# Kernel tuning notes

Hardware: AMD Instinct MI355X
Metric: run time of the kernel (lower is better)

The kernel has to match this reference:

```python
import jax, jax.numpy as jnp
import numpy as np

N = 1_000_000   # mesh points
D_IN = 5        # scalar invariants
H = 128         # hidden width
L = 5           # hidden layers
NB = 10         # tensor bases

# t0 generator basis rows (flattened 3x3 deviatoric diag tensors)
T01 = np.array([-1/3, 0, 0, 0, 1/6, 0, 0, 0, 1/6], dtype=np.float32)
T02 = np.array([1/6, 0, 0, 0, -1/3, 0, 0, 0, 1/6], dtype=np.float32)
T03 = np.array([1/6, 0, 0, 0, 1/6, 0, 0, 0, -1/3], dtype=np.float32)


def _linear_params(k, fan_in, fan_out):
    # xavier_uniform_ with gain=1.0, bias filled with 0.01 (as in init_w_and_b)
    limit = float(np.sqrt(6.0 / (fan_in + fan_out)))
    W = jax.random.uniform(k, (fan_in, fan_out), jnp.float32, -limit, limit)
    b = jnp.full((fan_out,), 0.01, jnp.float32)
    return W, b


def setup_inputs() -> dict:
    key = jax.random.key(0)
    ks = jax.random.split(key, 16)
    x = jax.random.normal(ks[0], (N, D_IN), jnp.float32)
    tb = jax.random.normal(ks[1], (N, NB, 9), jnp.float32)
    inp = {"x": x, "tb": tb}
    dims = [D_IN] + [H] * L
    for i in range(L):
        W, b = _linear_params(ks[2 + i], dims[i], dims[i + 1])
        inp[f"W{i+1}"] = W
        inp[f"b{i+1}"] = b
    inp["Wc"], inp["bc"] = _linear_params(ks[2 + L], H, NB)
    inp["Wg1"], inp["bg1"] = _linear_params(ks[3 + L], H, 1)
    inp["Wg2"], inp["bg2"] = _linear_params(ks[4 + L], H, 1)
    inp["Wg3"], inp["bg3"] = _linear_params(ks[5 + L], H, 1)
    return inp


def reference(x, tb, W1, b1, W2, b2, W3, b3, W4, b4, W5, b5,
              Wc, bc, Wg1, bg1, Wg2, bg2, Wg3, bg3):
    h = x
    for W, b in ((W1, b1), (W2, b2), (W3, b3), (W4, b4), (W5, b5)):
        h = jax.nn.relu(h @ W + b)          # [N, H]
    coeffs = h @ Wc + bc                     # [N, NB]
    g1 = h @ Wg1 + bg1                       # [N, 1]
    g2 = h @ Wg2 + bg2
    g3 = h @ Wg3 + bg3
    t0 = g1 * jnp.asarray(T01) + g2 * jnp.asarray(T02) + g3 * jnp.asarray(T03)  # [N, 9]
    # batched tensor-basis contraction replacing the per-point double loop
    bij = t0 + jnp.einsum('nt,ntc->nc', coeffs, tb)  # [N, 9]
    return bij
```

## Files before the change

### kernel.cpp

```cpp
#include <hip/hip_runtime.h>
#include <stdint.h>


#define NPTS   1000000
#define TPB    512
#define NBLKS  256
#define PTILE  256
#define NT     ((NPTS + PTILE - 1) / PTILE)

typedef uint32_t u32;
typedef __attribute__((ext_vector_type(4)))  u32   u32x4;
typedef __attribute__((ext_vector_type(8)))  short s16x8;
typedef __attribute__((ext_vector_type(16))) float f32x16;
typedef __attribute__((ext_vector_type(4), aligned(4))) float f32x4u;

#define WS_L(l)   ((l)*65536)
#define WS_TAIL   262144
#define WS_W1     (262144 + 8192)
#define WS_BIAS   (262144 + 12288)

#define LDS_BUF0   0
#define LDS_BUF1   65536
#define LDS_HEADS  131072
#define LDS_W1     (131072 + 8192)
#define LDS_BIAS   (131072 + 12288)
#define LDS_TOTAL  147456

#define MFMA(a,b,c) __builtin_amdgcn_mfma_f32_32x32x16_bf16((a),(b),(c),0,0,0)
#define BC16(v)     __builtin_bit_cast(s16x8, (v))

__device__ __forceinline__ u32 cvtpk(float lo, float hi) {
    u32 r;
    asm("v_cvt_pk_bf16_f32 %0, %1, %2" : "=v"(r) : "v"(lo), "v"(hi));
    return r;
}
__device__ __forceinline__ float lo2f(u32 p){ return __builtin_bit_cast(float, p << 16); }
__device__ __forceinline__ float hi2f(u32 p){ return __builtin_bit_cast(float, p & 0xffff0000u); }
__device__ __forceinline__ uint16_t f2bf(float f) {
    u32 u = __builtin_bit_cast(u32, f);
    return (uint16_t)((u + 0x7fffu + ((u >> 16) & 1u)) >> 16);
}
__device__ __forceinline__ float b2f(uint16_t h){ return __builtin_bit_cast(float, (u32)h << 16); }

__device__ __forceinline__ void stageN(const char* g, char* l, int tid, int nbytes) {
    const int w = tid >> 6, ln = tid & 63;
    const char* gp = g + w*1024 + ln*16;
    char* lp = l + w*1024;
    #pragma unroll
    for (int i = 0; i < 8; ++i) {
        if (i*8192 >= nbytes) break;
        __builtin_amdgcn_global_load_lds(
            (const __attribute__((address_space(1))) uint32_t*)(gp + i*8192),
            (__attribute__((address_space(3))) uint32_t*)(lp + i*8192), 16, 0, 0);
    }
}

extern "C" __global__ void __launch_bounds__(256)
tbnn_prep(const float* __restrict__ W1, const float* __restrict__ b1,
          const float* __restrict__ W2, const float* __restrict__ b2,
          const float* __restrict__ W3, const float* __restrict__ b3,
          const float* __restrict__ W4, const float* __restrict__ b4,
          const float* __restrict__ W5, const float* __restrict__ b5,
          const float* __restrict__ Wc, const float* __restrict__ bc,
          const float* __restrict__ Wg1,const float* __restrict__ bg1,
          const float* __restrict__ Wg2,const float* __restrict__ bg2,
          const float* __restrict__ Wg3,const float* __restrict__ bg3,
          char* __restrict__ ws)
{
    int idx = blockIdx.x*256 + threadIdx.x;
    if (idx < 65536) {
        int l = idx >> 14, r = idx & 16383, ifc = r >> 7, of = r & 127;
        const float* Wt = (l==0)?W2:(l==1)?W3:(l==2)?W4:W5;
        float w = Wt[ifc*128 + of];
        uint16_t hb = f2bf(w);
        uint16_t lb = f2bf(w - b2f(hb));
        char* row = ws + WS_L(l) + of*512;
        int o = (2*ifc) ^ ((of&15)<<4);
        *(uint16_t*)(row + o)       = hb;
        *(uint16_t*)(row + 256 + o) = lb;
    } else if (idx < 65536 + 2048) {
        int j = idx - 65536, of = j >> 7, ifc = j & 127;
        float v = 0.f;
        if      (of < 10)  v = Wc[ifc*10 + of];
        else if (of == 10) v = Wg1[ifc];
        else if (of == 11) v = Wg2[ifc];
        else if (of == 12) v = Wg3[ifc];
        uint16_t hb = f2bf(v);
        uint16_t lb = f2bf(v - b2f(hb));
        char* row = ws + WS_TAIL + of*512;
        int o = (2*ifc) ^ ((of&15)<<4);
        *(uint16_t*)(row + o)       = hb;
        *(uint16_t*)(row + 256 + o) = lb;
    } else if (idx < 65536 + 2048 + 128) {
        int of = idx - (65536 + 2048);
        uint16_t* dst = (uint16_t*)(ws + WS_W1 + of*32);
        #pragma unroll
        for (int s = 0; s < 5; ++s) {
            float w = W1[s*128 + of];
            uint16_t hb = f2bf(w);
            dst[s]      = hb;
            dst[6 + s]  = f2bf(w - b2f(hb));
            dst[11 + s] = hb;
        }
        dst[5] = f2bf(b1[of]);
    } else if (idx < 65536 + 2048 + 128 + 544) {
        int j = idx - (65536 + 2048 + 128);
        float v = 0.f;
        if (j < 512) {
            int l = j >> 7, of = j & 127;
            const float* bt = (l==0)?b2:(l==1)?b3:(l==2)?b4:b5;
            v = bt[of];
        } else {
            int of = j - 512;
            if      (of < 10)  v = bc[of];
            else if (of == 10) v = bg1[0];
            else if (of == 11) v = bg2[0];
            else if (of == 12) v = bg3[0];
        }
        *(uint16_t*)(ws + WS_BIAS + j*2) = f2bf(v);
    }
}

#define LAYER(lc, BUFOFF) do {                                                   \
    const char* wb = smem + (BUFOFF);                                            \
    __builtin_amdgcn_s_setprio(1);                                               \
    _Pragma("unroll")                                                            \
    for (int k = 0; k < 8; ++k) {                                                \
        int so = (k*32 + hib) ^ sm;                                              \
        const char* rp = wb + col*512 + so;                                      \
        u32x4 H0 = *(const u32x4*)(rp);                                          \
        u32x4 L0v = *(const u32x4*)(rp + 256);                                   \
        u32x4 H1 = *(const u32x4*)(rp + 32*512);                                 \
        u32x4 L1v = *(const u32x4*)(rp + 32*512 + 256);                          \
        u32x4 H2 = *(const u32x4*)(rp + 64*512);                                 \
        u32x4 L2v = *(const u32x4*)(rp + 64*512 + 256);                          \
        u32x4 H3 = *(const u32x4*)(rp + 96*512);                                 \
        u32x4 L3v = *(const u32x4*)(rp + 96*512 + 256);                          \
        s16x8 bl = BC16(Bl[k]), bh = BC16(Bh[k]);                                \
        acc[0] = MFMA(BC16(H0), bl, (k==0)?zf:acc[0]);                           \
        acc[1] = MFMA(BC16(H1), bl, (k==0)?zf:acc[1]);                           \
        acc[2] = MFMA(BC16(H2), bl, (k==0)?zf:acc[2]);                           \
        acc[3] = MFMA(BC16(H3), bl, (k==0)?zf:acc[3]);                           \
        acc[0] = MFMA(BC16(H0), bh, acc[0]);                                     \
        acc[1] = MFMA(BC16(H1), bh, acc[1]);                                     \
        acc[2] = MFMA(BC16(H2), bh, acc[2]);                                     \
        acc[3] = MFMA(BC16(H3), bh, acc[3]);                                     \
        acc[0] = MFMA(BC16(L0v), bh, acc[0]);                                    \
        acc[1] = MFMA(BC16(L1v), bh, acc[1]);                                    \
        acc[2] = MFMA(BC16(L2v), bh, acc[2]);                                    \
        acc[3] = MFMA(BC16(L3v), bh, acc[3]);                                    \
    }                                                                            \
    _Pragma("unroll")                                                            \
    for (int ot = 0; ot < 4; ++ot) {                                             \
        u32 bw = (u32)*(const uint16_t*)(smem + LDS_BIAS + ((lc)*128 + ot*32 + col)*2); \
        u32x4 Ab; Ab[0] = hi ? 0u : bw; Ab[1]=0u; Ab[2]=0u; Ab[3]=0u;            \
        acc[ot] = MFMA(BC16(Ab), BC16(Bc), acc[ot]);                             \
    }                                                                            \
    __builtin_amdgcn_s_setprio(0);                                               \
    convert();                                                                   \
} while (0)

extern "C" __global__ void __launch_bounds__(TPB)
tbnn_main(const float* __restrict__ x, const float* __restrict__ tb,
          const char* __restrict__ ws, float* __restrict__ out)
{
    extern __shared__ char smem[];
    const int tid  = threadIdx.x;
    const int wave = tid >> 6;
    const int lane = tid & 63;
    const int col  = lane & 31;
    const int hi   = lane >> 5;
    const int sm   = (col & 15) << 4;
    const int hib  = hi * 16;

    stageN(ws + WS_TAIL, smem + LDS_HEADS, tid, 16384);
    stageN(ws + WS_L(0), smem + LDS_BUF0,  tid, 65536);
    stageN(ws + WS_L(1), smem + LDS_BUF1,  tid, 65536);
    __syncthreads();

    u32x4 Bc; Bc[0] = hi ? 0u : 0x00003F80u; Bc[1]=0u; Bc[2]=0u; Bc[3]=0u;
    f32x16 zf;
    #pragma unroll
    for (int i = 0; i < 16; ++i) zf[i] = 0.f;

    for (int t = blockIdx.x; t < NT; t += gridDim.x) {
        const int pb = t*PTILE + wave*32;
        const int p  = pb + col;

        f32x16 acc[4];
        u32x4  Bh[8], Bl[8];

        auto convert = [&]() {
            #pragma unroll
            for (int ot = 0; ot < 4; ++ot) {
                f32x16 a = acc[ot];
                #pragma unroll
                for (int h2 = 0; h2 < 2; ++h2) {
                    float e0 = fmaxf(a[8*h2+0], 0.f), e1 = fmaxf(a[8*h2+1], 0.f);
                    float e2 = fmaxf(a[8*h2+2], 0.f), e3 = fmaxf(a[8*h2+3], 0.f);
                    float e4 = fmaxf(a[8*h2+4], 0.f), e5 = fmaxf(a[8*h2+5], 0.f);
                    float e6 = fmaxf(a[8*h2+6], 0.f), e7 = fmaxf(a[8*h2+7], 0.f);
                    u32 h01 = cvtpk(e0,e1), h23 = cvtpk(e2,e3);
                    u32 h45 = cvtpk(e4,e5), h67 = cvtpk(e6,e7);
                    u32 l01 = cvtpk(e0 - lo2f(h01), e1 - hi2f(h01));
                    u32 l23 = cvtpk(e2 - lo2f(h23), e3 - hi2f(h23));
                    u32 l45 = cvtpk(e4 - lo2f(h45), e5 - hi2f(h45));
                    u32 l67 = cvtpk(e6 - lo2f(h67), e7 - hi2f(h67));
                    auto sh1 = __builtin_amdgcn_permlane32_swap(h01, h45, false, false);
                    auto sh2 = __builtin_amdgcn_permlane32_swap(h23, h67, false, false);
                    u32x4 fh; fh[0]=sh1[0]; fh[1]=sh2[0]; fh[2]=sh1[1]; fh[3]=sh2[1];
                    Bh[2*ot+h2] = fh;
                    auto sl1 = __builtin_amdgcn_permlane32_swap(l01, l45, false, false);
                    auto sl2 = __builtin_amdgcn_permlane32_swap(l23, l67, false, false);
                    u32x4 fl; fl[0]=sl1[0]; fl[1]=sl2[0]; fl[2]=sl1[1]; fl[3]=sl2[1];
                    Bl[2*ot+h2] = fl;
                }
            }
        };

        {
            float x0=0.f,x1=0.f,x2=0.f,x3=0.f,x4=0.f;
            if (p < NPTS) {
                const float* xp = x + (size_t)p*5;
                f32x4u v = *(const f32x4u*)xp;
                x0=v.x; x1=v.y; x2=v.z; x3=v.w; x4=xp[4];
            }
            float h0 = lo2f(cvtpk(x0,x0)), l0 = x0 - h0;
            float h1 = lo2f(cvtpk(x1,x1)), l1 = x1 - h1;
            float h2 = lo2f(cvtpk(x2,x2)), l2 = x2 - h2;
            float h3 = lo2f(cvtpk(x3,x3)), l3 = x3 - h3;
            float h4 = lo2f(cvtpk(x4,x4)), l4 = x4 - h4;
            u32x4 Bx;
            if (hi == 0) {
                Bx[0] = cvtpk(h0,h1); Bx[1] = cvtpk(h2,h3);
                Bx[2] = cvtpk(h4,1.0f); Bx[3] = cvtpk(h0,h1);
            } else {
                Bx[0] = cvtpk(h2,h3); Bx[1] = cvtpk(h4,l0);
                Bx[2] = cvtpk(l1,l2); Bx[3] = cvtpk(l3,l4);
            }
            #pragma unroll
            for (int ot = 0; ot < 4; ++ot) {
                u32x4 Av = *(const u32x4*)(smem + LDS_W1 + (ot*32+col)*32 + hib);
                acc[ot] = MFMA(BC16(Av), BC16(Bx), zf);
            }
        }
        convert();

        LAYER(0, LDS_BUF0);
        __syncthreads();
        stageN(ws + WS_L(2), smem + LDS_BUF0, tid, 65536);
        LAYER(1, LDS_BUF1);
        __syncthreads();
        stageN(ws + WS_L(3), smem + LDS_BUF1, tid, 65536);
        LAYER(2, LDS_BUF0);
        __syncthreads();
        stageN(ws + WS_L(0), smem + LDS_BUF0, tid, 65536);
        LAYER(3, LDS_BUF1);
        __syncthreads();
        stageN(ws + WS_L(1), smem + LDS_BUF1, tid, 65536);

        f32x16 hA, hB;
        __builtin_amdgcn_s_setprio(1);
        #pragma unroll
        for (int k = 0; k < 8; ++k) {
            int so = (k*32 + hib) ^ sm;
            const char* rp = smem + LDS_HEADS + (col&15)*512;
            u32x4 HH = *(const u32x4*)(rp + so);
            u32x4 HL = *(const u32x4*)(rp + 256 + so);
            s16x8 bl = BC16(Bl[k]), bh = BC16(Bh[k]);
            if (k & 1) {
                hB = MFMA(BC16(HH), bl, (k==1)?zf:hB);
                hB = MFMA(BC16(HH), bh, hB);
                hB = MFMA(BC16(HL), bh, hB);
            } else {
                hA = MFMA(BC16(HH), bl, (k==0)?zf:hA);
                hA = MFMA(BC16(HH), bh, hA);
                hA = MFMA(BC16(HL), bh, hA);
            }
        }
        {
            u32 bw = (u32)*(const uint16_t*)(smem + LDS_BIAS + (512 + col)*2);
            u32x4 Ab; Ab[0] = hi ? 0u : bw; Ab[1]=0u; Ab[2]=0u; Ab[3]=0u;
            hA = MFMA(BC16(Ab), BC16(Bc), hA);
        }
        __builtin_amdgcn_s_setprio(0);
        f32x16 h6 = hA + hB;

        if (p < NPTS) {
            const float* tbp = tb + (size_t)p*90;
            f32x16 c = h6;
            const float sixth = 0.16666666666666666f;
            const float third = 0.3333333333333333f;
            float s[9];
            if (hi == 0) {
                float g1 = c[6], g2 = c[7];
                s[0] = -g1*third + g2*sixth;
                s[4] =  g1*sixth - g2*third;
                s[8] =  g1*sixth + g2*sixth;
            } else {
                float g3 = c[4];
                s[0] =  g3*sixth;
                s[4] =  g3*sixth;
                s[8] = -g3*third;
            }
            s[1]=s[2]=s[3]=s[5]=s[6]=s[7]=0.f;
            #pragma unroll
            for (int j = 0; j < 4; ++j) {
                int trow = (hi ? 4 : 0) + j;
                float cf = c[j];
                const float* r = tbp + trow*9;
                f32x4u r0 = *(const f32x4u*)(r);
                f32x4u r1 = *(const f32x4u*)(r + 4);
                float r8 = r[8];
                s[0] += cf*r0.x; s[1] += cf*r0.y; s[2] += cf*r0.z; s[3] += cf*r0.w;
                s[4] += cf*r1.x; s[5] += cf*r1.y; s[6] += cf*r1.z; s[7] += cf*r1.w;
                s[8] += cf*r8;
            }
            if (hi == 0) {
                #pragma unroll
                for (int j = 4; j < 6; ++j) {
                    int trow = 4 + j;
                    float cf = c[j];
                    const float* r = tbp + trow*9;
                    f32x4u r0 = *(const f32x4u*)(r);
                    f32x4u r1 = *(const f32x4u*)(r + 4);
                    float r8 = r[8];
                    s[0] += cf*r0.x; s[1] += cf*r0.y; s[2] += cf*r0.z; s[3] += cf*r0.w;
                    s[4] += cf*r1.x; s[5] += cf*r1.y; s[6] += cf*r1.z; s[7] += cf*r1.w;
                    s[8] += cf*r8;
                }
            }
            #pragma unroll
            for (int j = 0; j < 9; ++j) {
                u32 uv = __builtin_bit_cast(u32, s[j]);
                auto rr = __builtin_amdgcn_permlane32_swap(uv, uv, false, false);
                s[j] = __builtin_bit_cast(float, (u32)rr[0]) + __builtin_bit_cast(float, (u32)rr[1]);
            }
            if (hi == 0) {
                float* op = out + (size_t)p*9;
                f32x4u o0, o1;
                o0.x=s[0]; o0.y=s[1]; o0.z=s[2]; o0.w=s[3];
                o1.x=s[4]; o1.y=s[5]; o1.z=s[6]; o1.w=s[7];
                *(f32x4u*)op       = o0;
                *(f32x4u*)(op + 4) = o1;
                op[8] = s[8];
            }
        }
    }
    __syncthreads();
}

extern "C" void kernel_launch(void* const* d_in, const int* in_sizes, int n_in,
                              void* d_out, int out_size, void* d_ws, size_t ws_size,
                              hipStream_t stream) {
    (void)in_sizes; (void)n_in; (void)out_size; (void)ws_size;
    char* ws = (char*)d_ws;
    hipLaunchKernelGGL(tbnn_prep, dim3(267), dim3(256), 0, stream,
        (const float*)d_in[2],  (const float*)d_in[3],
        (const float*)d_in[4],  (const float*)d_in[5],
        (const float*)d_in[6],  (const float*)d_in[7],
        (const float*)d_in[8],  (const float*)d_in[9],
        (const float*)d_in[10], (const float*)d_in[11],
        (const float*)d_in[12], (const float*)d_in[13],
        (const float*)d_in[14], (const float*)d_in[15],
        (const float*)d_in[16], (const float*)d_in[17],
        (const float*)d_in[18], (const float*)d_in[19],
        ws);
    (void)hipFuncSetAttribute((const void*)tbnn_main,
                              hipFuncAttributeMaxDynamicSharedMemorySize, LDS_TOTAL);
    hipLaunchKernelGGL(tbnn_main, dim3(NBLKS), dim3(TPB), LDS_TOTAL, stream,
        (const float*)d_in[0], (const float*)d_in[1], ws, (float*)d_out);
}
```

Measured before the change: 413.3 us.

## Process two 32-point sub-tiles per wave to amortize weight restaging

Each wave now handles 64 points per tile (two 32-point groups with separate bf16 hi/lo activation buffers), doubling PTILE to 512. Every staged layer weight buffer is reused across both groups, so the per-tile global-to-LDS restaging of all four 64KB hidden-layer weights and the matching barriers happen half as often per point. The heads GEMM also drops its two-accumulator split and uses a single chain. In exchange, register pressure roughly doubles for the activation operands, which may cause spills or lower occupancy at 512 threads per block.

```diff
diff --git a/kernel.cpp b/kernel.cpp
--- a/kernel.cpp
+++ b/kernel.cpp
@@ -5,7 +5,7 @@
 #define NPTS   1000000
 #define TPB    512
 #define NBLKS  256
-#define PTILE  256
+#define PTILE  512
 #define NT     ((NPTS + PTILE - 1) / PTILE)
 
 typedef uint32_t u32;
@@ -121,45 +121,6 @@
     }
 }
 
-#define LAYER(lc, BUFOFF) do {                                                   \
-    const char* wb = smem + (BUFOFF);                                            \
-    __builtin_amdgcn_s_setprio(1);                                               \
-    _Pragma("unroll")                                                            \
-    for (int k = 0; k < 8; ++k) {                                                \
-        int so = (k*32 + hib) ^ sm;                                              \
-        const char* rp = wb + col*512 + so;                                      \
-        u32x4 H0 = *(const u32x4*)(rp);                                          \
-        u32x4 L0v = *(const u32x4*)(rp + 256);                                   \
-        u32x4 H1 = *(const u32x4*)(rp + 32*512);                                 \
-        u32x4 L1v = *(const u32x4*)(rp + 32*512 + 256);                          \
-        u32x4 H2 = *(const u32x4*)(rp + 64*512);                                 \
-        u32x4 L2v = *(const u32x4*)(rp + 64*512 + 256);                          \
-        u32x4 H3 = *(const u32x4*)(rp + 96*512);                                 \
-        u32x4 L3v = *(const u32x4*)(rp + 96*512 + 256);                          \
-        s16x8 bl = BC16(Bl[k]), bh = BC16(Bh[k]);                                \
-        acc[0] = MFMA(BC16(H0), bl, (k==0)?zf:acc[0]);                           \
-        acc[1] = MFMA(BC16(H1), bl, (k==0)?zf:acc[1]);                           \
-        acc[2] = MFMA(BC16(H2), bl, (k==0)?zf:acc[2]);                           \
-        acc[3] = MFMA(BC16(H3), bl, (k==0)?zf:acc[3]);                           \
-        acc[0] = MFMA(BC16(H0), bh, acc[0]);                                     \
-        acc[1] = MFMA(BC16(H1), bh, acc[1]);                                     \
-        acc[2] = MFMA(BC16(H2), bh, acc[2]);                                     \
-        acc[3] = MFMA(BC16(H3), bh, acc[3]);                                     \
-        acc[0] = MFMA(BC16(L0v), bh, acc[0]);                                    \
-        acc[1] = MFMA(BC16(L1v), bh, acc[1]);                                    \
-        acc[2] = MFMA(BC16(L2v), bh, acc[2]);                                    \
-        acc[3] = MFMA(BC16(L3v), bh, acc[3]);                                    \
-    }                                                                            \
-    _Pragma("unroll")                                                            \
-    for (int ot = 0; ot < 4; ++ot) {                                             \
-        u32 bw = (u32)*(const uint16_t*)(smem + LDS_BIAS + ((lc)*128 + ot*32 + col)*2); \
-        u32x4 Ab; Ab[0] = hi ? 0u : bw; Ab[1]=0u; Ab[2]=0u; Ab[3]=0u;            \
-        acc[ot] = MFMA(BC16(Ab), BC16(Bc), acc[ot]);                             \
-    }                                                                            \
-    __builtin_amdgcn_s_setprio(0);                                               \
-    convert();                                                                   \
-} while (0)
-
 extern "C" __global__ void __launch_bounds__(TPB)
 tbnn_main(const float* __restrict__ x, const float* __restrict__ tb,
           const char* __restrict__ ws, float* __restrict__ out)
@@ -183,130 +144,152 @@
     #pragma unroll
     for (int i = 0; i < 16; ++i) zf[i] = 0.f;
 
-    for (int t = blockIdx.x; t < NT; t += gridDim.x) {
-        const int pb = t*PTILE + wave*32;
-        const int p  = pb + col;
-
-        f32x16 acc[4];
-        u32x4  Bh[8], Bl[8];
-
-        auto convert = [&]() {
+    f32x16 acc[4];
+    u32x4  B1h[8], B1l[8], B2h[8], B2l[8];
+
+    auto convert = [&](u32x4* BH, u32x4* BL) {
+        #pragma unroll
+        for (int ot = 0; ot < 4; ++ot) {
+            f32x16 a = acc[ot];
             #pragma unroll
-            for (int ot = 0; ot < 4; ++ot) {
-                f32x16 a = acc[ot];
-                #pragma unroll
-                for (int h2 = 0; h2 < 2; ++h2) {
-                    float e0 = fmaxf(a[8*h2+0], 0.f), e1 = fmaxf(a[8*h2+1], 0.f);
-                    float e2 = fmaxf(a[8*h2+2], 0.f), e3 = fmaxf(a[8*h2+3], 0.f);
-                    float e4 = fmaxf(a[8*h2+4], 0.f), e5 = fmaxf(a[8*h2+5], 0.f);
-                    float e6 = fmaxf(a[8*h2+6], 0.f), e7 = fmaxf(a[8*h2+7], 0.f);
-                    u32 h01 = cvtpk(e0,e1), h23 = cvtpk(e2,e3);
-                    u32 h45 = cvtpk(e4,e5), h67 = cvtpk(e6,e7);
-                    u32 l01 = cvtpk(e0 - lo2f(h01), e1 - hi2f(h01));
-                    u32 l23 = cvtpk(e2 - lo2f(h23), e3 - hi2f(h23));
-                    u32 l45 = cvtpk(e4 - lo2f(h45), e5 - hi2f(h45));
-                    u32 l67 = cvtpk(e6 - lo2f(h67), e7 - hi2f(h67));
-                    auto sh1 = __builtin_amdgcn_permlane32_swap(h01, h45, false, false);
-                    auto sh2 = __builtin_amdgcn_permlane32_swap(h23, h67, false, false);
-                    u32x4 fh; fh[0]=sh1[0]; fh[1]=sh2[0]; fh[2]=sh1[1]; fh[3]=sh2[1];
-                    Bh[2*ot+h2] = fh;
-                    auto sl1 = __builtin_amdgcn_permlane32_swap(l01, l45, false, false);
-                    auto sl2 = __builtin_amdgcn_permlane32_swap(l23, l67, false, false);
-                    u32x4 fl; fl[0]=sl1[0]; fl[1]=sl2[0]; fl[2]=sl1[1]; fl[3]=sl2[1];
-                    Bl[2*ot+h2] = fl;
-                }
+            for (int h2 = 0; h2 < 2; ++h2) {
+                float e0 = fmaxf(a[8*h2+0], 0.f), e1 = fmaxf(a[8*h2+1], 0.f);
+                float e2 = fmaxf(a[8*h2+2], 0.f), e3 = fmaxf(a[8*h2+3], 0.f);
+                float e4 = fmaxf(a[8*h2+4], 0.f), e5 = fmaxf(a[8*h2+5], 0.f);
+                float e6 = fmaxf(a[8*h2+6], 0.f), e7 = fmaxf(a[8*h2+7], 0.f);
+                u32 h01 = cvtpk(e0,e1), h23 = cvtpk(e2,e3);
+                u32 h45 = cvtpk(e4,e5), h67 = cvtpk(e6,e7);
+                u32 l01 = cvtpk(e0 - lo2f(h01), e1 - hi2f(h01));
+                u32 l23 = cvtpk(e2 - lo2f(h23), e3 - hi2f(h23));
+                u32 l45 = cvtpk(e4 - lo2f(h45), e5 - hi2f(h45));
+                u32 l67 = cvtpk(e6 - lo2f(h67), e7 - hi2f(h67));
+                auto sh1 = __builtin_amdgcn_permlane32_swap(h01, h45, false, false);
+                auto sh2 = __builtin_amdgcn_permlane32_swap(h23, h67, false, false);
+                u32x4 fh; fh[0]=sh1[0]; fh[1]=sh2[0]; fh[2]=sh1[1]; fh[3]=sh2[1];
+                BH[2*ot+h2] = fh;
+                auto sl1 = __builtin_amdgcn_permlane32_swap(l01, l45, false, false);
+                auto sl2 = __builtin_amdgcn_permlane32_swap(l23, l67, false, false);
+                u32x4 fl; fl[0]=sl1[0]; fl[1]=sl2[0]; fl[2]=sl1[1]; fl[3]=sl2[1];
+                BL[2*ot+h2] = fl;
             }
-        };
-
-        {
-            float x0=0.f,x1=0.f,x2=0.f,x3=0.f,x4=0.f;
-            if (p < NPTS) {
-                const float* xp = x + (size_t)p*5;
-                f32x4u v = *(const f32x4u*)xp;
-                x0=v.x; x1=v.y; x2=v.z; x3=v.w; x4=xp[4];
-            }
-            float h0 = lo2f(cvtpk(x0,x0)), l0 = x0 - h0;
-            float h1 = lo2f(cvtpk(x1,x1)), l1 = x1 - h1;
-            float h2 = lo2f(cvtpk(x2,x2)), l2 = x2 - h2;
-            float h3 = lo2f(cvtpk(x3,x3)), l3 = x3 - h3;
-            float h4 = lo2f(cvtpk(x4,x4)), l4 = x4 - h4;
-            u32x4 Bx;
-            if (hi == 0) {
-                Bx[0] = cvtpk(h0,h1); Bx[1] = cvtpk(h2,h3);
-                Bx[2] = cvtpk(h4,1.0f); Bx[3] = cvtpk(h0,h1);
-            } else {
-                Bx[0] = cvtpk(h2,h3); Bx[1] = cvtpk(h4,l0);
-                Bx[2] = cvtpk(l1,l2); Bx[3] = cvtpk(l3,l4);
-            }
-            #pragma unroll
-            for (int ot = 0; ot < 4; ++ot) {
-                u32x4 Av = *(const u32x4*)(smem + LDS_W1 + (ot*32+col)*32 + hib);
-                acc[ot] = MFMA(BC16(Av), BC16(Bx), zf);
-            }
-        }
-        convert();
-
-        LAYER(0, LDS_BUF0);
-        __syncthreads();
-        stageN(ws + WS_L(2), smem + LDS_BUF0, tid, 65536);
-        LAYER(1, LDS_BUF1);
-        __syncthreads();
-        stageN(ws + WS_L(3), smem + LDS_BUF1, tid, 65536);
-        LAYER(2, LDS_BUF0);
-        __syncthreads();
-        stageN(ws + WS_L(0), smem + LDS_BUF0, tid, 65536);
-        LAYER(3, LDS_BUF1);
-        __syncthreads();
-        stageN(ws + WS_L(1), smem + LDS_BUF1, tid, 65536);
-
-        f32x16 hA, hB;
-        __builtin_amdgcn_s_setprio(1);
+        }
+    };
+
+    auto l1 = [&](int p) {
+        float x0=0.f,x1=0.f,x2=0.f,x3=0.f,x4=0.f;
+        if (p < NPTS) {
+            const float* xp = x + (size_t)p*5;
+            f32x4u v = *(const f32x4u*)xp;
+            x0=v.x; x1=v.y; x2=v.z; x3=v.w; x4=xp[4];
+        }
+        float h0 = lo2f(cvtpk(x0,x0)), l0 = x0 - h0;
+        float h1 = lo2f(cvtpk(x1,x1)), l1v = x1 - h1;
+        float h2 = lo2f(cvtpk(x2,x2)), l2 = x2 - h2;
+        float h3 = lo2f(cvtpk(x3,x3)), l3 = x3 - h3;
+        float h4 = lo2f(cvtpk(x4,x4)), l4 = x4 - h4;
+        u32x4 Bx;
+        if (hi == 0) {
+            Bx[0] = cvtpk(h0,h1); Bx[1] = cvtpk(h2,h3);
+            Bx[2] = cvtpk(h4,1.0f); Bx[3] = cvtpk(h0,h1);
+        } else {
+            Bx[0] = cvtpk(h2,h3); Bx[1] = cvtpk(h4,l0);
+            Bx[2] = cvtpk(l1v,l2); Bx[3] = cvtpk(l3,l4);
+        }
+        #pragma unroll
+        for (int ot = 0; ot < 4; ++ot) {
+            u32x4 Av = *(const u32x4*)(smem + LDS_W1 + (ot*32+col)*32 + hib);
+            acc[ot] = MFMA(BC16(Av), BC16(Bx), zf);
+        }
+    };
+
+    auto kloop = [&](const char* wb, const u32x4* BH, const u32x4* BL) {
+        #pragma unroll
+        for (int k = 0; k < 8; ++k) {
+            int so = (k*32 + hib) ^ sm;
+            const char* rp = wb + col*512 + so;
+            u32x4 H0 = *(const u32x4*)(rp);
+            u32x4 L0v = *(const u32x4*)(rp + 256);
+            u32x4 H1 = *(const u32x4*)(rp + 32*512);
+            u32x4 L1v = *(const u32x4*)(rp + 32*512 + 256);
+            u32x4 H2 = *(const u32x4*)(rp + 64*512);
+            u32x4 L2v = *(const u32x4*)(rp + 64*512 + 256);
+            u32x4 H3 = *(const u32x4*)(rp + 96*512);
+            u32x4 L3v = *(const u32x4*)(rp + 96*512 + 256);
+            s16x8 bl = BC16(BL[k]), bh = BC16(BH[k]);
+            acc[0] = MFMA(BC16(H0), bl, (k==0)?zf:acc[0]);
+            acc[1] = MFMA(BC16(H1), bl, (k==0)?zf:acc[1]);
+            acc[2] = MFMA(BC16(H2), bl, (k==0)?zf:acc[2]);
+            acc[3] = MFMA(BC16(H3), bl, (k==0)?zf:acc[3]);
+            acc[0] = MFMA(BC16(H0), bh, acc[0]);
+            acc[1] = MFMA(BC16(H1), bh, acc[1]);
+            acc[2] = MFMA(BC16(H2), bh, acc[2]);
+            acc[3] = MFMA(BC16(H3), bh, acc[3]);
+            acc[0] = MFMA(BC16(L0v), bh, acc[0]);
+            acc[1] = MFMA(BC16(L1v), bh, acc[1]);
+            acc[2] = MFMA(BC16(L2v), bh, acc[2]);
+            acc[3] = MFMA(BC16(L3v), bh, acc[3]);
+        }
+    };
+    auto biask = [&](int lc) {
+        #pragma unroll
+        for (int ot = 0; ot < 4; ++ot) {
+            u32 bw = (u32)*(const uint16_t*)(smem + LDS_BIAS + (lc*128 + ot*32 + col)*2);
+            u32x4 Ab; Ab[0] = hi ? 0u : bw; Ab[1]=0u; Ab[2]=0u; Ab[3]=0u;
+            acc[ot] = MFMA(BC16(Ab), BC16(Bc), acc[ot]);
+        }
+    };
+
+    auto headsg = [&](const u32x4* BH, const u32x4* BL) -> f32x16 {
+        f32x16 h6;
         #pragma unroll
         for (int k = 0; k < 8; ++k) {
             int so = (k*32 + hib) ^ sm;
             const char* rp = smem + LDS_HEADS + (col&15)*512;
             u32x4 HH = *(const u32x4*)(rp + so);
             u32x4 HL = *(const u32x4*)(rp + 256 + so);
-            s16x8 bl = BC16(Bl[k]), bh = BC16(Bh[k]);
-            if (k & 1) {
-                hB = MFMA(BC16(HH), bl, (k==1)?zf:hB);
-                hB = MFMA(BC16(HH), bh, hB);
-                hB = MFMA(BC16(HL), bh, hB);
-            } else {
-                hA = MFMA(BC16(HH), bl, (k==0)?zf:hA);
-                hA = MFMA(BC16(HH), bh, hA);
-                hA = MFMA(BC16(HL), bh, hA);
-            }
-        }
-        {
-            u32 bw = (u32)*(const uint16_t*)(smem + LDS_BIAS + (512 + col)*2);
-            u32x4 Ab; Ab[0] = hi ? 0u : bw; Ab[1]=0u; Ab[2]=0u; Ab[3]=0u;
-            hA = MFMA(BC16(Ab), BC16(Bc), hA);
-        }
-        __builtin_amdgcn_s_setprio(0);
-        f32x16 h6 = hA + hB;
-
-        if (p < NPTS) {
-            const float* tbp = tb + (size_t)p*90;
-            f32x16 c = h6;
-            const float sixth = 0.16666666666666666f;
-            const float third = 0.3333333333333333f;
-            float s[9];
-            if (hi == 0) {
-                float g1 = c[6], g2 = c[7];
-                s[0] = -g1*third + g2*sixth;
-                s[4] =  g1*sixth - g2*third;
-                s[8] =  g1*sixth + g2*sixth;
-            } else {
-                float g3 = c[4];
-                s[0] =  g3*sixth;
-                s[4] =  g3*sixth;
-                s[8] = -g3*third;
-            }
-            s[1]=s[2]=s[3]=s[5]=s[6]=s[7]=0.f;
+            h6 = MFMA(BC16(HH), BC16(BL[k]), (k==0)?zf:h6);
+            h6 = MFMA(BC16(HH), BC16(BH[k]), h6);
+            h6 = MFMA(BC16(HL), BC16(BH[k]), h6);
+        }
+        u32 bw = (u32)*(const uint16_t*)(smem + LDS_BIAS + (512 + col)*2);
+        u32x4 Ab; Ab[0] = hi ? 0u : bw; Ab[1]=0u; Ab[2]=0u; Ab[3]=0u;
+        return MFMA(BC16(Ab), BC16(Bc), h6);
+    };
+
+    auto contraction = [&](int p, f32x16 c) {
+        if (p >= NPTS) return;
+        const float* tbp = tb + (size_t)p*90;
+        const float sixth = 0.16666666666666666f;
+        const float third = 0.3333333333333333f;
+        float s[9];
+        if (hi == 0) {
+            float g1 = c[6], g2 = c[7];
+            s[0] = -g1*third + g2*sixth;
+            s[4] =  g1*sixth - g2*third;
+            s[8] =  g1*sixth + g2*sixth;
+        } else {
+            float g3 = c[4];
+            s[0] =  g3*sixth;
+            s[4] =  g3*sixth;
+            s[8] = -g3*third;
+        }
+        s[1]=s[2]=s[3]=s[5]=s[6]=s[7]=0.f;
+        #pragma unroll
+        for (int j = 0; j < 4; ++j) {
+            int trow = (hi ? 4 : 0) + j;
+            float cf = c[j];
+            const float* r = tbp + trow*9;
+            f32x4u r0 = *(const f32x4u*)(r);
+            f32x4u r1 = *(const f32x4u*)(r + 4);
+            float r8 = r[8];
+            s[0] += cf*r0.x; s[1] += cf*r0.y; s[2] += cf*r0.z; s[3] += cf*r0.w;
+            s[4] += cf*r1.x; s[5] += cf*r1.y; s[6] += cf*r1.z; s[7] += cf*r1.w;
+            s[8] += cf*r8;
+        }
+        if (hi == 0) {
             #pragma unroll
-            for (int j = 0; j < 4; ++j) {
-                int trow = (hi ? 4 : 0) + j;
+            for (int j = 4; j < 6; ++j) {
+                int trow = 4 + j;
                 float cf = c[j];
                 const float* r = tbp + trow*9;
                 f32x4u r0 = *(const f32x4u*)(r);
@@ -316,36 +299,68 @@
                 s[4] += cf*r1.x; s[5] += cf*r1.y; s[6] += cf*r1.z; s[7] += cf*r1.w;
                 s[8] += cf*r8;
             }
-            if (hi == 0) {
-                #pragma unroll
-                for (int j = 4; j < 6; ++j) {
-                    int trow = 4 + j;
-                    float cf = c[j];
-                    const float* r = tbp + trow*9;
-                    f32x4u r0 = *(const f32x4u*)(r);
-                    f32x4u r1 = *(const f32x4u*)(r + 4);
-                    float r8 = r[8];
-                    s[0] += cf*r0.x; s[1] += cf*r0.y; s[2] += cf*r0.z; s[3] += cf*r0.w;
-                    s[4] += cf*r1.x; s[5] += cf*r1.y; s[6] += cf*r1.z; s[7] += cf*r1.w;
-                    s[8] += cf*r8;
-                }
-            }
-            #pragma unroll
-            for (int j = 0; j < 9; ++j) {
-                u32 uv = __builtin_bit_cast(u32, s[j]);
-                auto rr = __builtin_amdgcn_permlane32_swap(uv, uv, false, false);
-                s[j] = __builtin_bit_cast(float, (u32)rr[0]) + __builtin_bit_cast(float, (u32)rr[1]);
-            }
-            if (hi == 0) {
-                float* op = out + (size_t)p*9;
-                f32x4u o0, o1;
-                o0.x=s[0]; o0.y=s[1]; o0.z=s[2]; o0.w=s[3];
-                o1.x=s[4]; o1.y=s[5]; o1.z=s[6]; o1.w=s[7];
-                *(f32x4u*)op       = o0;
-                *(f32x4u*)(op + 4) = o1;
-                op[8] = s[8];
-            }
-        }
+        }
+        #pragma unroll
+        for (int j = 0; j < 9; ++j) {
+            u32 uv = __builtin_bit_cast(u32, s[j]);
+            auto rr = __builtin_amdgcn_permlane32_swap(uv, uv, false, false);
+            s[j] = __builtin_bit_cast(float, (u32)rr[0]) + __builtin_bit_cast(float, (u32)rr[1]);
+        }
+        if (hi == 0) {
+            float* op = out + (size_t)p*9;
+            f32x4u o0, o1;
+            o0.x=s[0]; o0.y=s[1]; o0.z=s[2]; o0.w=s[3];
+            o1.x=s[4]; o1.y=s[5]; o1.z=s[6]; o1.w=s[7];
+            *(f32x4u*)op       = o0;
+            *(f32x4u*)(op + 4) = o1;
+            op[8] = s[8];
+        }
+    };
+
+    for (int t = blockIdx.x; t < NT; t += gridDim.x) {
+        const int p1 = t*PTILE + wave*64 + col;
+        const int p2 = p1 + 32;
+
+        l1(p1); convert(B1h, B1l);
+        l1(p2); convert(B2h, B2l);
+        __syncthreads();
+
+        __builtin_amdgcn_s_setprio(1); kloop(smem + LDS_BUF0, B1h, B1l); biask(0); __builtin_amdgcn_s_setprio(0);
+        convert(B1h, B1l);
+        __builtin_amdgcn_s_setprio(1); kloop(smem + LDS_BUF0, B2h, B2l); biask(0); __builtin_amdgcn_s_setprio(0);
+        convert(B2h, B2l);
+        __syncthreads();
+        stageN(ws + WS_L(2), smem + LDS_BUF0, tid, 65536);
+
+        __builtin_amdgcn_s_setprio(1); kloop(smem + LDS_BUF1, B1h, B1l); biask(1); __builtin_amdgcn_s_setprio(0);
+        convert(B1h, B1l);
+        __builtin_amdgcn_s_setprio(1); kloop(smem + LDS_BUF1, B2h, B2l); biask(1); __builtin_amdgcn_s_setprio(0);
+        convert(B2h, B2l);
+        __syncthreads();
+        stageN(ws + WS_L(3), smem + LDS_BUF1, tid, 65536);
+
+        __builtin_amdgcn_s_setprio(1); kloop(smem + LDS_BUF0, B1h, B1l); biask(2); __builtin_amdgcn_s_setprio(0);
+        convert(B1h, B1l);
+        __builtin_amdgcn_s_setprio(1); kloop(smem + LDS_BUF0, B2h, B2l); biask(2); __builtin_amdgcn_s_setprio(0);
+        convert(B2h, B2l);
+        __syncthreads();
+        stageN(ws + WS_L(0), smem + LDS_BUF0, tid, 65536);
+
+        __builtin_amdgcn_s_setprio(1); kloop(smem + LDS_BUF1, B1h, B1l); biask(3); __builtin_amdgcn_s_setprio(0);
+        convert(B1h, B1l);
+        __builtin_amdgcn_s_setprio(1); kloop(smem + LDS_BUF1, B2h, B2l); biask(3); __builtin_amdgcn_s_setprio(0);
+        convert(B2h, B2l);
+        __syncthreads();
+        stageN(ws + WS_L(1), smem + LDS_BUF1, tid, 65536);
+
+        __builtin_amdgcn_s_setprio(1);
+        f32x16 h6a = headsg(B1h, B1l);
+        __builtin_amdgcn_s_setprio(0);
+        contraction(p1, h6a);
+        __builtin_amdgcn_s_setprio(1);
+        f32x16 h6b = headsg(B2h, B2l);
+        __builtin_amdgcn_s_setprio(0);
+        contraction(p2, h6b);
     }
     __syncthreads();
 }
```

Result: slower. 479.1 us (+15.9%).
